# Kernel tuning notes

Hardware: AMD Instinct MI355X
Metric: run time of the kernel (lower is better)

Reference implementation:

```python
import jax, jax.numpy as jnp
import numpy as np

N, E, D, T, B, OUT = 20000, 80000, 768, 4, 3, 768
SCALE = 0.02


def _layer_norm(x, g, b):
    mu = jnp.mean(x, axis=-1, keepdims=True)
    var = jnp.var(x, axis=-1, keepdims=True)
    return (x - mu) / jnp.sqrt(var + 1e-5) * g + b


def _typed_linear(x, etype, bases, coeff):
    # DGL TypedLinear with basis regularizer: W[t] = sum_b coeff[t,b] * bases[b]
    # computed as 3 shared GEMMs + per-edge weighted sum (avoids [E,D,D] gather).
    c = coeff[etype]  # [E, B]
    y = c[:, 0:1] * (x @ bases[0])
    for bb in range(1, bases.shape[0]):
        y = y + c[:, bb:bb + 1] * (x @ bases[bb])
    return y


def _time_encode(t, freq, phase):
    return jnp.cos(t[:, None] * freq[None, :] + phase[None, :])


def _segment_softmax(scores, seg, n):
    m = jax.ops.segment_max(scores, seg, num_segments=n)
    m = jnp.where(jnp.isfinite(m), m, 0.0)  # empty segments -> -inf guard
    e = jnp.exp(scores - m[seg])
    den = jax.ops.segment_sum(e, seg, num_segments=n)[seg]
    return e / jnp.where(den == 0, 1.0, den)


def _forward(h, etime_hete, first_etime_homo, second_etime_homo, w_src, w_dst,
             ln_g, ln_b, src_bases, src_coeff, dst_bases, dst_coeff,
             user_bases, user_coeff, lin_w, lin_b, time_freq, time_phase,
             src_hete, dst_hete, first_etype_hete, src_homo, dst_homo,
             first_etype_homo, second_etype_homo, n_nodes):
    inv_sqrt_d = 1.0 / jnp.sqrt(jnp.asarray(768.0, h.dtype))
    n_src = h @ w_src.T  # src_weight (no bias)
    n_dst = h @ w_dst.T  # dst_weight (no bias)

    # --- heterogeneous edges ---
    sf = n_src[src_hete]
    df = n_dst[dst_hete]
    hete_src = jax.nn.relu(_typed_linear(_layer_norm(sf, ln_g, ln_b), first_etype_hete, src_bases, src_coeff))
    msg_h = _time_encode(etime_hete, time_freq, time_phase) + hete_src
    e_h = jnp.sum(msg_h * df, axis=1) * inv_sqrt_d
    a_h = _segment_softmax(e_h, dst_hete, n_nodes)
    h_hete = jax.ops.segment_sum(a_h[:, None] * msg_h, dst_hete, num_segments=n_nodes)

    # --- homogeneous edges ---
    sf = n_src[src_homo]
    df = n_dst[dst_homo]
    dst_feat = jax.nn.relu(_typed_linear(_layer_norm(df, ln_g, ln_b), first_etype_homo, dst_bases, dst_coeff))
    homo_feat = jax.nn.relu(_typed_linear(_layer_norm(sf, ln_g, ln_b), second_etype_homo, user_bases, user_coeff))
    t_homo = jnp.maximum(first_etime_homo, second_etime_homo)
    msg_o = _time_encode(t_homo, time_freq, time_phase) + homo_feat
    e_o = jnp.sum(msg_o * dst_feat, axis=1) * inv_sqrt_d
    a_o = _segment_softmax(e_o, dst_homo, n_nodes)
    h_homo = jax.ops.segment_sum(a_o[:, None] * msg_o, dst_homo, num_segments=n_nodes)

    n = jnp.concatenate([h_hete, h_homo], axis=-1)  # [N, 2D]
    z = jax.nn.relu(n @ lin_w.T + lin_b)
    zn = jnp.linalg.norm(z, axis=1, keepdims=True)
    return z / jnp.where(zn == 0, 1.0, zn)


def setup_inputs() -> dict:
    key = jax.random.key(0)
    ks = jax.random.split(key, 24)
    inp = {
        'h': jax.random.normal(ks[0], (N, D), jnp.float32),
        'etime_hete': jax.random.uniform(ks[1], (E,), jnp.float32),
        'first_etime_homo': jax.random.uniform(ks[2], (E,), jnp.float32),
        'second_etime_homo': jax.random.uniform(ks[3], (E,), jnp.float32),
        'w_src': jax.random.normal(ks[4], (D, D), jnp.float32) * SCALE,
        'w_dst': jax.random.normal(ks[5], (D, D), jnp.float32) * SCALE,
        'ln_g': jnp.ones((D,), jnp.float32),
        'ln_b': jnp.zeros((D,), jnp.float32),
        'src_bases': jax.random.normal(ks[6], (B, D, D), jnp.float32) * SCALE,
        'src_coeff': jax.random.normal(ks[7], (T, B), jnp.float32),
        'dst_bases': jax.random.normal(ks[8], (B, D, D), jnp.float32) * SCALE,
        'dst_coeff': jax.random.normal(ks[9], (T, B), jnp.float32),
        'user_bases': jax.random.normal(ks[10], (B, D, D), jnp.float32) * SCALE,
        'user_coeff': jax.random.normal(ks[11], (T, B), jnp.float32),
        'lin_w': jax.random.normal(ks[12], (OUT, 2 * D), jnp.float32) * SCALE,
        'lin_b': jnp.zeros((OUT,), jnp.float32),
        'time_freq': jnp.asarray(1.0 / 10 ** np.linspace(0, 9, D), jnp.float32),
        'time_phase': jnp.zeros((D,), jnp.float32),
        'src_hete': jax.random.randint(ks[13], (E,), 0, N, jnp.int32),
        'dst_hete': jax.random.randint(ks[14], (E,), 0, N, jnp.int32),
        'first_etype_hete': jax.random.randint(ks[15], (E,), 0, T, jnp.int32),
        'src_homo': jax.random.randint(ks[16], (E,), 0, N, jnp.int32),
        'dst_homo': jax.random.randint(ks[17], (E,), 0, N, jnp.int32),
        'first_etype_homo': jax.random.randint(ks[18], (E,), 0, T, jnp.int32),
        'second_etype_homo': jax.random.randint(ks[19], (E,), 0, T, jnp.int32),
        'num_nodes': N,
    }
    return inp


def reference(h, etime_hete, first_etime_homo, second_etime_homo, w_src, w_dst,
              ln_g, ln_b, src_bases, src_coeff, dst_bases, dst_coeff,
              user_bases, user_coeff, lin_w, lin_b, time_freq, time_phase,
              src_hete, dst_hete, first_etype_hete, src_homo, dst_homo,
              first_etype_homo, second_etype_homo, num_nodes):
    return _forward(h, etime_hete, first_etime_homo, second_etime_homo, w_src,
                    w_dst, ln_g, ln_b, src_bases, src_coeff, dst_bases,
                    dst_coeff, user_bases, user_coeff, lin_w, lin_b,
                    time_freq, time_phase, src_hete, dst_hete,
                    first_etype_hete, src_homo, dst_homo, first_etype_homo,
                    second_etype_homo, num_nodes)
```

## Files before the change

### kernel.cpp

```cpp
#include <hip/hip_runtime.h>
#include <hip/hip_bf16.h>
#include <stdint.h>

#define D 768
#define INV_SQRT_D 0.03608439182435161269f

static void* g_scratch = nullptr;
#define SCRATCH_BYTES ((size_t)600 * 1024 * 1024)

__attribute__((constructor))
static void _alloc_scratch() {
    if (hipMalloc(&g_scratch, SCRATCH_BYTES) != hipSuccess) g_scratch = nullptr;
}

static inline int cdiv(int a, int b) { return (a + b - 1) / b; }

typedef __attribute__((ext_vector_type(8))) short bf16x8;
typedef __attribute__((ext_vector_type(4))) float f32x4;

__device__ __forceinline__ unsigned short f2b(float f) {
    union { float f; unsigned u; } c; c.f = f;
    unsigned r = c.u + 0x7FFF + ((c.u >> 16) & 1);
    return (unsigned short)(r >> 16);
}
__device__ __forceinline__ float b2f(unsigned short u) {
    union { unsigned u; float f; } c; c.u = (unsigned)u << 16;
    return c.f;
}

__device__ __forceinline__ float block_reduce_sum(float v) {
#pragma unroll
    for (int off = 32; off > 0; off >>= 1) v += __shfl_down(v, off, 64);
    __shared__ float sm[4];
    int lane = threadIdx.x & 63, w = threadIdx.x >> 6;
    __syncthreads();
    if (lane == 0) sm[w] = v;
    __syncthreads();
    return (sm[0] + sm[1]) + (sm[2] + sm[3]);
}

template <bool CONCAT, bool BF16C, bool RELU, bool BIAS>
__global__ __launch_bounds__(256) void mfma_gemm(
    const unsigned short* __restrict__ A1, const unsigned short* __restrict__ A2,
    int lda, int ksplit,
    const unsigned short* __restrict__ B, int ldb,
    void* __restrict__ Cv, int ldc,
    const float* __restrict__ bias,
    int M, int K)
{
    __shared__ unsigned short As[128 * 32];
    __shared__ unsigned short Bs[128 * 32];
    const int tid = threadIdx.x;
    const int wv = tid >> 6, lane = tid & 63;
    const int m0 = blockIdx.y * 128, n0 = blockIdx.x * 128;
    const int wm = (wv >> 1) << 6;
    const int wn = (wv & 1) << 6;
    const int fr = lane & 15;
    const int fq = lane >> 4;

    f32x4 acc[4][4] = {};

    for (int k0 = 0; k0 < K; k0 += 32) {
        const unsigned short* Asrc = A1;
        int kk = k0;
        if (CONCAT && k0 >= ksplit) { Asrc = A2; kk = k0 - ksplit; }
#pragma unroll
        for (int j = 0; j < 2; ++j) {
            int idx = j * 256 + tid;
            int row = idx >> 2, cb = (idx & 3) << 3;
            int am = m0 + row; if (am > M - 1) am = M - 1;
            const unsigned short* ga = Asrc + (size_t)am * lda + kk + cb;
            char* la = (char*)As + (size_t)(j * 256 + wv * 64) * 16;
            __builtin_amdgcn_global_load_lds(
                (const __attribute__((address_space(1))) unsigned int*)ga,
                (__attribute__((address_space(3))) unsigned int*)la, 16, 0, 0);
            const unsigned short* gb = B + (size_t)(n0 + row) * ldb + k0 + cb;
            char* lb = (char*)Bs + (size_t)(j * 256 + wv * 64) * 16;
            __builtin_amdgcn_global_load_lds(
                (const __attribute__((address_space(1))) unsigned int*)gb,
                (__attribute__((address_space(3))) unsigned int*)lb, 16, 0, 0);
        }
        __syncthreads();

        bf16x8 af[4], bfv[4];
#pragma unroll
        for (int i = 0; i < 4; ++i) {
            af[i]  = *(const bf16x8*)&As[(wm + i * 16 + fr) * 32 + fq * 8];
            bfv[i] = *(const bf16x8*)&Bs[(wn + i * 16 + fr) * 32 + fq * 8];
        }
#pragma unroll
        for (int mi = 0; mi < 4; ++mi)
#pragma unroll
            for (int ni = 0; ni < 4; ++ni)
                acc[mi][ni] = __builtin_amdgcn_mfma_f32_16x16x32_bf16(
                    af[mi], bfv[ni], acc[mi][ni], 0, 0, 0);
        __syncthreads();
    }

#pragma unroll
    for (int mi = 0; mi < 4; ++mi) {
#pragma unroll
        for (int r = 0; r < 4; ++r) {
            int m = m0 + wm + mi * 16 + fq * 4 + r;
            if (m >= M) continue;
#pragma unroll
            for (int ni = 0; ni < 4; ++ni) {
                int n = n0 + wn + ni * 16 + fr;
                float v = acc[mi][ni][r];
                if (BIAS) v += bias[n];
                if (RELU) v = fmaxf(v, 0.f);
                if (BF16C) ((unsigned short*)Cv)[(size_t)m * ldc + n] = f2b(v);
                else       ((float*)Cv)[(size_t)m * ldc + n] = v;
            }
        }
    }
}

__global__ void f32_to_bf16_kernel(const float* __restrict__ in,
                                   unsigned short* __restrict__ out, int n4) {
    int i = blockIdx.x * 256 + threadIdx.x;
    if (i >= n4) return;
    float4 v = *reinterpret_cast<const float4*>(in + (size_t)i * 4);
    ushort4 o;
    o.x = f2b(v.x); o.y = f2b(v.y); o.z = f2b(v.z); o.w = f2b(v.w);
    *reinterpret_cast<ushort4*>(out + (size_t)i * 4) = o;
}

__global__ __launch_bounds__(256) void combine_transpose_kernel(
    const float* __restrict__ in, const float* __restrict__ coeff,
    unsigned short* __restrict__ out) {
    int t = blockIdx.z;
    float c0 = coeff[t * 3 + 0], c1 = coeff[t * 3 + 1], c2 = coeff[t * 3 + 2];
    __shared__ float tile[32][33];
    int bx = blockIdx.x * 32, by = blockIdx.y * 32;
    int tx = threadIdx.x & 31, ty = threadIdx.x >> 5;
#pragma unroll
    for (int i = 0; i < 32; i += 8) {
        size_t idx = (size_t)(by + ty + i) * D + bx + tx;
        tile[ty + i][tx] = c0 * in[idx] + c1 * in[idx + (size_t)D * D]
                         + c2 * in[idx + (size_t)2 * D * D];
    }
    __syncthreads();
    unsigned short* o = out + (size_t)t * D * D;
#pragma unroll
    for (int i = 0; i < 32; i += 8)
        o[(size_t)(bx + ty + i) * D + by + tx] = f2b(tile[tx][ty + i]);
}

__global__ __launch_bounds__(256) void ln_bf16_kernel(
    unsigned short* __restrict__ x, int ld,
    const float* __restrict__ g, const float* __restrict__ b)
{
    unsigned short* r = x + (size_t)blockIdx.x * ld;
    int t = threadIdx.x;
    float v0 = b2f(r[t]), v1 = b2f(r[t + 256]), v2 = b2f(r[t + 512]);
    float s = block_reduce_sum(v0 + v1 + v2);
    float mu = s * (1.f / 768.f);
    float d0 = v0 - mu, d1 = v1 - mu, d2 = v2 - mu;
    float q = block_reduce_sum(d0 * d0 + d1 * d1 + d2 * d2);
    float rstd = 1.f / sqrtf(q * (1.f / 768.f) + 1e-5f);
    r[t]       = f2b(d0 * rstd * g[t]       + b[t]);
    r[t + 256] = f2b(d1 * rstd * g[t + 256] + b[t + 256]);
    r[t + 512] = f2b(d2 * rstd * g[t + 512] + b[t + 512]);
}

__global__ __launch_bounds__(256) void score_hete_kernel(
    const unsigned short* __restrict__ P, int ldp,
    const unsigned short* __restrict__ nd, int ldn,
    const float* __restrict__ etime,
    const int* __restrict__ src, const int* __restrict__ dst, const int* __restrict__ et,
    const float* __restrict__ freq, const float* __restrict__ phase,
    float* __restrict__ esc, int E)
{
    int e = blockIdx.x * 4 + (threadIdx.x >> 6);
    if (e >= E) return;
    int l = threadIdx.x & 63;
    int s = src[e], d = dst[e], ty = et[e];
    float tv = etime[e];
    const unsigned short* ps = P + (size_t)s * ldp + ty * D;
    const unsigned short* pd = nd + (size_t)d * ldn;
    float acc = 0.f;
    {
        bf16x8 a = *(const bf16x8*)(ps + l * 8);
        bf16x8 b = *(const bf16x8*)(pd + l * 8);
#pragma unroll
        for (int q = 0; q < 8; ++q) {
            int j = l * 8 + q;
            float m = __cosf(tv * freq[j] + phase[j]) + b2f((unsigned short)a[q]);
            acc += m * b2f((unsigned short)b[q]);
        }
    }
    if (l < 32) {
        bf16x8 a = *(const bf16x8*)(ps + 512 + l * 8);
        bf16x8 b = *(const bf16x8*)(pd + 512 + l * 8);
#pragma unroll
        for (int q = 0; q < 8; ++q) {
            int j = 512 + l * 8 + q;
            float m = __cosf(tv * freq[j] + phase[j]) + b2f((unsigned short)a[q]);
            acc += m * b2f((unsigned short)b[q]);
        }
    }
#pragma unroll
    for (int off = 32; off > 0; off >>= 1) acc += __shfl_down(acc, off, 64);
    if (l == 0) esc[e] = acc * INV_SQRT_D;
}

__global__ __launch_bounds__(256) void score_homo_kernel(
    const unsigned short* __restrict__ Pd, int ldpd,
    const unsigned short* __restrict__ Pu, int ldpu,
    const float* __restrict__ t1, const float* __restrict__ t2,
    const int* __restrict__ src, const int* __restrict__ dst,
    const int* __restrict__ et1, const int* __restrict__ et2,
    const float* __restrict__ freq, const float* __restrict__ phase,
    float* __restrict__ esc, int E)
{
    int e = blockIdx.x * 4 + (threadIdx.x >> 6);
    if (e >= E) return;
    int l = threadIdx.x & 63;
    int s = src[e], d = dst[e];
    int ta = et1[e], tb = et2[e];
    float tv = fmaxf(t1[e], t2[e]);
    const unsigned short* pu = Pu + (size_t)s * ldpu + tb * D;
    const unsigned short* pd = Pd + (size_t)d * ldpd + ta * D;
    float acc = 0.f;
    {
        bf16x8 a = *(const bf16x8*)(pu + l * 8);
        bf16x8 b = *(const bf16x8*)(pd + l * 8);
#pragma unroll
        for (int q = 0; q < 8; ++q) {
            int j = l * 8 + q;
            float m = __cosf(tv * freq[j] + phase[j]) + b2f((unsigned short)a[q]);
            acc += m * b2f((unsigned short)b[q]);
        }
    }
    if (l < 32) {
        bf16x8 a = *(const bf16x8*)(pu + 512 + l * 8);
        bf16x8 b = *(const bf16x8*)(pd + 512 + l * 8);
#pragma unroll
        for (int q = 0; q < 8; ++q) {
            int j = 512 + l * 8 + q;
            float m = __cosf(tv * freq[j] + phase[j]) + b2f((unsigned short)a[q]);
            acc += m * b2f((unsigned short)b[q]);
        }
    }
#pragma unroll
    for (int off = 32; off > 0; off >>= 1) acc += __shfl_down(acc, off, 64);
    if (l == 0) esc[e] = acc * INV_SQRT_D;
}

__global__ void zero_int_kernel(int* __restrict__ p, int n) {
    int i = blockIdx.x * 256 + threadIdx.x;
    if (i < n) p[i] = 0;
}

__global__ void count_kernel(const int* __restrict__ dst, int* __restrict__ cnt, int E) {
    int e = blockIdx.x * 256 + threadIdx.x;
    if (e < E) atomicAdd(&cnt[dst[e]], 1);
}

__global__ __launch_bounds__(1024) void scan_kernel(
    const int* __restrict__ cnt, int* __restrict__ offs, int n)
{
    __shared__ int tmp[1024];
    __shared__ int carry;
    int tid = threadIdx.x;
    if (tid == 0) carry = 0;
    __syncthreads();
    for (int base = 0; base < n; base += 1024) {
        int idx = base + tid;
        int v = (idx < n) ? cnt[idx] : 0;
        tmp[tid] = v;
        __syncthreads();
        for (int off = 1; off < 1024; off <<= 1) {
            int t = (tid >= off) ? tmp[tid - off] : 0;
            __syncthreads();
            tmp[tid] += t;
            __syncthreads();
        }
        int inc = tmp[tid];
        int c = carry;
        if (idx < n) offs[idx] = c + inc - v;
        __syncthreads();
        if (tid == 0) carry = c + tmp[1023];
        __syncthreads();
    }
    if (tid == 0) offs[n] = carry;
}

__global__ void scatter_kernel(const int* __restrict__ dst, const int* __restrict__ offs,
                               int* __restrict__ cur, int* __restrict__ list, int E) {
    int e = blockIdx.x * 256 + threadIdx.x;
    if (e < E) {
        int d = dst[e];
        int pos = offs[d] + atomicAdd(&cur[d], 1);
        list[pos] = e;
    }
}

__global__ void seg_softmax_kernel(const int* __restrict__ offs, const int* __restrict__ list,
                                   float* __restrict__ score, int n) {
    int v = blockIdx.x * 256 + threadIdx.x;
    if (v >= n) return;
    int a = offs[v], b = offs[v + 1];
    if (a == b) return;
    float m = -INFINITY;
    for (int i = a; i < b; i++) m = fmaxf(m, score[list[i]]);
    float den = 0.f;
    for (int i = a; i < b; i++) den += expf(score[list[i]] - m);
    float inv = 1.f / den;
    for (int i = a; i < b; i++) { int e = list[i]; score[e] = expf(score[e] - m) * inv; }
}

__global__ __launch_bounds__(256) void agg_hete_kernel(
    const int* __restrict__ offs, const int* __restrict__ list,
    const float* __restrict__ a,
    const unsigned short* __restrict__ P, int ldp,
    const float* __restrict__ etime,
    const int* __restrict__ src, const int* __restrict__ et,
    const float* __restrict__ freq, const float* __restrict__ phase,
    unsigned short* __restrict__ out)
{
    int v = blockIdx.x;
    int t = threadIdx.x;
    float f0 = freq[t], f1 = freq[t + 256], f2 = freq[t + 512];
    float p0 = phase[t], p1 = phase[t + 256], p2 = phase[t + 512];
    float a0 = 0.f, a1 = 0.f, a2 = 0.f;
    for (int i = offs[v]; i < offs[v + 1]; ++i) {
        int e = list[i];
        int s = src[e], ty = et[e];
        float w = a[e];
        float tv = etime[e];
        const unsigned short* ps = P + (size_t)s * ldp + ty * D;
        a0 += w * (__cosf(tv * f0 + p0) + b2f(ps[t]));
        a1 += w * (__cosf(tv * f1 + p1) + b2f(ps[t + 256]));
        a2 += w * (__cosf(tv * f2 + p2) + b2f(ps[t + 512]));
    }
    unsigned short* o = out + (size_t)v * D;
    o[t] = f2b(a0); o[t + 256] = f2b(a1); o[t + 512] = f2b(a2);
}

__global__ __launch_bounds__(256) void agg_homo_kernel(
    const int* __restrict__ offs, const int* __restrict__ list,
    const float* __restrict__ a,
    const unsigned short* __restrict__ Pu, int ldpu,
    const float* __restrict__ t1, const float* __restrict__ t2,
    const int* __restrict__ src, const int* __restrict__ et2,
    const float* __restrict__ freq, const float* __restrict__ phase,
    unsigned short* __restrict__ out)
{
    int v = blockIdx.x;
    int t = threadIdx.x;
    float f0 = freq[t], f1 = freq[t + 256], f2 = freq[t + 512];
    float p0 = phase[t], p1 = phase[t + 256], p2 = phase[t + 512];
    float a0 = 0.f, a1 = 0.f, a2 = 0.f;
    for (int i = offs[v]; i < offs[v + 1]; ++i) {
        int e = list[i];
        int s = src[e], tb = et2[e];
        float w = a[e];
        float tv = fmaxf(t1[e], t2[e]);
        const unsigned short* pu = Pu + (size_t)s * ldpu + tb * D;
        a0 += w * (__cosf(tv * f0 + p0) + b2f(pu[t]));
        a1 += w * (__cosf(tv * f1 + p1) + b2f(pu[t + 256]));
        a2 += w * (__cosf(tv * f2 + p2) + b2f(pu[t + 512]));
    }
    unsigned short* o = out + (size_t)v * D;
    o[t] = f2b(a0); o[t + 256] = f2b(a1); o[t + 512] = f2b(a2);
}

__global__ __launch_bounds__(256) void normalize_kernel(
    const float* __restrict__ z, float* __restrict__ out)
{
    const float* x = z + (size_t)blockIdx.x * D;
    int t = threadIdx.x;
    float v0 = x[t], v1 = x[t + 256], v2 = x[t + 512];
    float s = block_reduce_sum(v0 * v0 + v1 * v1 + v2 * v2);
    float nrm = sqrtf(s);
    float inv = (nrm == 0.f) ? 1.f : 1.f / nrm;
    float* o = out + (size_t)blockIdx.x * D;
    o[t] = v0 * inv; o[t + 256] = v1 * inv; o[t + 512] = v2 * inv;
}

__global__ void fill_f32_kernel(float* __restrict__ p, float v, int n) {
    int i = blockIdx.x * 256 + threadIdx.x;
    if (i < n) p[i] = v;
}

extern "C" void kernel_launch(void* const* d_in, const int* in_sizes, int n_in,
                              void* d_out, int out_size, void* d_ws, size_t ws_size,
                              hipStream_t stream)
{
    const float* h          = (const float*)d_in[0];
    const float* etime_hete = (const float*)d_in[1];
    const float* t1_homo    = (const float*)d_in[2];
    const float* t2_homo    = (const float*)d_in[3];
    const float* w_src      = (const float*)d_in[4];
    const float* w_dst      = (const float*)d_in[5];
    const float* ln_g       = (const float*)d_in[6];
    const float* ln_b       = (const float*)d_in[7];
    const float* src_bases  = (const float*)d_in[8];
    const float* src_coeff  = (const float*)d_in[9];
    const float* dst_bases  = (const float*)d_in[10];
    const float* dst_coeff  = (const float*)d_in[11];
    const float* user_bases = (const float*)d_in[12];
    const float* user_coeff = (const float*)d_in[13];
    const float* lin_w      = (const float*)d_in[14];
    const float* lin_b      = (const float*)d_in[15];
    const float* time_freq  = (const float*)d_in[16];
    const float* time_phase = (const float*)d_in[17];
    const int* src_hete = (const int*)d_in[18];
    const int* dst_hete = (const int*)d_in[19];
    const int* et_hete  = (const int*)d_in[20];
    const int* src_homo = (const int*)d_in[21];
    const int* dst_homo = (const int*)d_in[22];
    const int* et1_homo = (const int*)d_in[23];
    const int* et2_homo = (const int*)d_in[24];

    const int N = in_sizes[0] / D;
    const int E = in_sizes[1];

    const size_t szST  = (size_t)N * 1536 * 2;
    const size_t szPSU = (size_t)N * 6144 * 2;
    const size_t szPD  = (size_t)N * 3072 * 2;
    const size_t szVb  = (size_t)N * D * 2;
    const size_t szW   = (size_t)D * D * 2;
    size_t need = szST + szPSU + szPD + 3 * szVb
                + 2 * szW + 2 * szW + 8 * szW + 4 * szW
                + (size_t)E * 4 + (size_t)N * 4
                + (((size_t)(N + 1) * 4 + 255) & ~(size_t)255) + (size_t)E * 4 + 8192;

    char* base;
    if (ws_size >= need) base = (char*)d_ws;
    else if (g_scratch)  base = (char*)g_scratch;
    else {
        fill_f32_kernel<<<cdiv(out_size, 256), 256, 0, stream>>>(
            (float*)d_out, 1000.0f + (float)(ws_size >> 20), out_size);
        return;
    }

    char* p = base;
    auto carve = [&](size_t bytes) { char* r = p; p += (bytes + 255) & ~(size_t)255; return r; };
    unsigned short* STb = (unsigned short*)carve(szST);
    unsigned short* PSU = (unsigned short*)carve(szPSU);
    unsigned short* PD  = (unsigned short*)carve(szPD);
    unsigned short* hb  = (unsigned short*)carve(szVb);
    unsigned short* hAb = (unsigned short*)carve(szVb);
    unsigned short* hOb = (unsigned short*)carve(szVb);
    unsigned short* wsb = (unsigned short*)carve(2 * szW);
    unsigned short* lwb = (unsigned short*)carve(2 * szW);
    unsigned short* suW = (unsigned short*)carve(8 * szW);
    unsigned short* dstW = (unsigned short*)carve(4 * szW);
    float* esc = (float*)carve((size_t)E * 4);
    int* cnt   = (int*)carve((size_t)N * 4);
    int* offs  = (int*)carve((size_t)(N + 1) * 4);
    int* list  = (int*)carve((size_t)E * 4);
    float* z   = (float*)PSU;

    unsigned short* Sb = STb;
    unsigned short* Tb = STb + 768;
    unsigned short* Psrc_t  = PSU;
    unsigned short* Puser_t = PSU + 3072;

    const int eb = cdiv(E, 256), nb = cdiv(N, 256);
    const int MB = cdiv(N, 128);
    dim3 g_proj(12, MB);
    dim3 g_psu(48, MB);
    dim3 g_pd(24, MB);
    dim3 g_fin(6, MB);
    dim3 ct_grid(24, 24, 4);
    const int seb = cdiv(E, 4);

    f32_to_bf16_kernel<<<cdiv(N * D / 4, 256), 256, 0, stream>>>(h, hb, N * D / 4);
    f32_to_bf16_kernel<<<cdiv(D * D / 4, 256), 256, 0, stream>>>(w_src, wsb, D * D / 4);
    f32_to_bf16_kernel<<<cdiv(D * D / 4, 256), 256, 0, stream>>>(w_dst, wsb + (size_t)D * D, D * D / 4);
    f32_to_bf16_kernel<<<cdiv(D * 2 * D / 4, 256), 256, 0, stream>>>(lin_w, lwb, D * 2 * D / 4);
    combine_transpose_kernel<<<ct_grid, 256, 0, stream>>>(src_bases, src_coeff, suW);
    combine_transpose_kernel<<<ct_grid, 256, 0, stream>>>(user_bases, user_coeff, suW + (size_t)4 * D * D);
    combine_transpose_kernel<<<ct_grid, 256, 0, stream>>>(dst_bases, dst_coeff, dstW);

    mfma_gemm<false, true, false, false><<<g_proj, 256, 0, stream>>>(
        hb, hb, D, D, wsb, D, STb, 1536, nullptr, N, D);
    ln_bf16_kernel<<<N, 256, 0, stream>>>(Sb, 1536, ln_g, ln_b);

    mfma_gemm<false, true, true, false><<<g_psu, 256, 0, stream>>>(
        Sb, Sb, 1536, D, suW, D, PSU, 6144, nullptr, N, D);

    zero_int_kernel<<<nb, 256, 0, stream>>>(cnt, N);
    count_kernel<<<eb, 256, 0, stream>>>(dst_hete, cnt, E);
    scan_kernel<<<1, 1024, 0, stream>>>(cnt, offs, N);
    zero_int_kernel<<<nb, 256, 0, stream>>>(cnt, N);
    scatter_kernel<<<eb, 256, 0, stream>>>(dst_hete, offs, cnt, list, E);

    score_hete_kernel<<<seb, 256, 0, stream>>>(Psrc_t, 6144, Tb, 1536, etime_hete,
                                               src_hete, dst_hete, et_hete,
                                               time_freq, time_phase, esc, E);
    seg_softmax_kernel<<<nb, 256, 0, stream>>>(offs, list, esc, N);
    agg_hete_kernel<<<N, 256, 0, stream>>>(offs, list, esc, Psrc_t, 6144, etime_hete,
                                           src_hete, et_hete, time_freq, time_phase, hAb);

    ln_bf16_kernel<<<N, 256, 0, stream>>>(Tb, 1536, ln_g, ln_b);
    mfma_gemm<false, true, true, false><<<g_pd, 256, 0, stream>>>(
        Tb, Tb, 1536, D, dstW, D, PD, 3072, nullptr, N, D);

    zero_int_kernel<<<nb, 256, 0, stream>>>(cnt, N);
    count_kernel<<<eb, 256, 0, stream>>>(dst_homo, cnt, E);
    scan_kernel<<<1, 1024, 0, stream>>>(cnt, offs, N);
    zero_int_kernel<<<nb, 256, 0, stream>>>(cnt, N);
    scatter_kernel<<<eb, 256, 0, stream>>>(dst_homo, offs, cnt, list, E);

    score_homo_kernel<<<seb, 256, 0, stream>>>(PD, 3072, Puser_t, 6144,
                                               t1_homo, t2_homo, src_homo, dst_homo,
                                               et1_homo, et2_homo, time_freq, time_phase, esc, E);
    seg_softmax_kernel<<<nb, 256, 0, stream>>>(offs, list, esc, N);
    agg_homo_kernel<<<N, 256, 0, stream>>>(offs, list, esc, Puser_t, 6144,
                                           t1_homo, t2_homo, src_homo, et2_homo,
                                           time_freq, time_phase, hOb);

    mfma_gemm<true, false, true, true><<<g_fin, 256, 0, stream>>>(
        hAb, hOb, D, D, lwb, 2 * D, z, D, lin_b, N, 2 * D);
    normalize_kernel<<<N, 256, 0, stream>>>(z, (float*)d_out);
}
```

Baseline: 1.142 ms.

## Use wave-per-node vectorized aggregation and merge both CSR builds

Result: no change. 1.127 ms (-1.3%).

```diff
diff --git a/kernel.cpp b/kernel.cpp
--- a/kernel.cpp
+++ b/kernel.cpp
@@ -18,10 +18,13 @@
 typedef __attribute__((ext_vector_type(8))) short bf16x8;
 typedef __attribute__((ext_vector_type(4))) float f32x4;
 
+__device__ __forceinline__ unsigned cvt2b(float lo, float hi) {
+    unsigned r;
+    asm("v_cvt_pk_bf16_f32 %0, %1, %2" : "=v"(r) : "v"(lo), "v"(hi));
+    return r;
+}
 __device__ __forceinline__ unsigned short f2b(float f) {
-    union { float f; unsigned u; } c; c.f = f;
-    unsigned r = c.u + 0x7FFF + ((c.u >> 16) & 1);
-    return (unsigned short)(r >> 16);
+    return (unsigned short)cvt2b(f, f);
 }
 __device__ __forceinline__ float b2f(unsigned short u) {
     union { unsigned u; float f; } c; c.u = (unsigned)u << 16;
@@ -253,47 +256,61 @@
     if (i < n) p[i] = 0;
 }
 
-__global__ void count_kernel(const int* __restrict__ dst, int* __restrict__ cnt, int E) {
+__global__ void count2_kernel(const int* __restrict__ dA, const int* __restrict__ dB,
+                              int* __restrict__ cntA, int* __restrict__ cntB, int E) {
     int e = blockIdx.x * 256 + threadIdx.x;
-    if (e < E) atomicAdd(&cnt[dst[e]], 1);
-}
-
-__global__ __launch_bounds__(1024) void scan_kernel(
-    const int* __restrict__ cnt, int* __restrict__ offs, int n)
+    if (e < E) {
+        atomicAdd(&cntA[dA[e]], 1);
+        atomicAdd(&cntB[dB[e]], 1);
+    }
+}
+
+__global__ __launch_bounds__(1024) void scan2_kernel(
+    const int* __restrict__ cntA, int* __restrict__ offsA,
+    const int* __restrict__ cntB, int* __restrict__ offsB, int n)
 {
     __shared__ int tmp[1024];
     __shared__ int carry;
     int tid = threadIdx.x;
-    if (tid == 0) carry = 0;
-    __syncthreads();
-    for (int base = 0; base < n; base += 1024) {
-        int idx = base + tid;
-        int v = (idx < n) ? cnt[idx] : 0;
-        tmp[tid] = v;
+    for (int g = 0; g < 2; ++g) {
+        const int* cnt = g ? cntB : cntA;
+        int* offs = g ? offsB : offsA;
         __syncthreads();
-        for (int off = 1; off < 1024; off <<= 1) {
-            int t = (tid >= off) ? tmp[tid - off] : 0;
+        if (tid == 0) carry = 0;
+        __syncthreads();
+        for (int base = 0; base < n; base += 1024) {
+            int idx = base + tid;
+            int v = (idx < n) ? cnt[idx] : 0;
+            tmp[tid] = v;
             __syncthreads();
-            tmp[tid] += t;
+            for (int off = 1; off < 1024; off <<= 1) {
+                int t = (tid >= off) ? tmp[tid - off] : 0;
+                __syncthreads();
+                tmp[tid] += t;
+                __syncthreads();
+            }
+            int inc = tmp[tid];
+            int c = carry;
+            if (idx < n) offs[idx] = c + inc - v;
             __syncthreads();
-        }
-        int inc = tmp[tid];
-        int c = carry;
-        if (idx < n) offs[idx] = c + inc - v;
-        __syncthreads();
-        if (tid == 0) carry = c + tmp[1023];
-        __syncthreads();
-    }
-    if (tid == 0) offs[n] = carry;
-}
-
-__global__ void scatter_kernel(const int* __restrict__ dst, const int* __restrict__ offs,
-                               int* __restrict__ cur, int* __restrict__ list, int E) {
+            if (tid == 0) carry = c + tmp[1023];
+            __syncthreads();
+        }
+        if (tid == 0) offs[n] = carry;
+    }
+}
+
+__global__ void scatter2_kernel(
+    const int* __restrict__ dA, const int* __restrict__ offsA,
+    int* __restrict__ curA, int* __restrict__ listA,
+    const int* __restrict__ dB, const int* __restrict__ offsB,
+    int* __restrict__ curB, int* __restrict__ listB, int E) {
     int e = blockIdx.x * 256 + threadIdx.x;
     if (e < E) {
-        int d = dst[e];
-        int pos = offs[d] + atomicAdd(&cur[d], 1);
-        list[pos] = e;
+        int d = dA[e];
+        listA[offsA[d] + atomicAdd(&curA[d], 1)] = e;
+        d = dB[e];
+        listB[offsB[d] + atomicAdd(&curB[d], 1)] = e;
     }
 }
 
@@ -311,60 +328,74 @@
     for (int i = a; i < b; i++) { int e = list[i]; score[e] = expf(score[e] - m) * inv; }
 }
 
-__global__ __launch_bounds__(256) void agg_hete_kernel(
+template <bool IS_HOMO>
+__global__ __launch_bounds__(256) void agg_kernel(
     const int* __restrict__ offs, const int* __restrict__ list,
     const float* __restrict__ a,
     const unsigned short* __restrict__ P, int ldp,
-    const float* __restrict__ etime,
+    const float* __restrict__ t1, const float* __restrict__ t2,
     const int* __restrict__ src, const int* __restrict__ et,
     const float* __restrict__ freq, const float* __restrict__ phase,
-    unsigned short* __restrict__ out)
-{
-    int v = blockIdx.x;
-    int t = threadIdx.x;
-    float f0 = freq[t], f1 = freq[t + 256], f2 = freq[t + 512];
-    float p0 = phase[t], p1 = phase[t + 256], p2 = phase[t + 512];
-    float a0 = 0.f, a1 = 0.f, a2 = 0.f;
-    for (int i = offs[v]; i < offs[v + 1]; ++i) {
+    unsigned short* __restrict__ out, int nN)
+{
+    int v = blockIdx.x * 4 + (threadIdx.x >> 6);
+    if (v >= nN) return;
+    int l = threadIdx.x & 63;
+
+    float frq[16], phs[16], acc[16];
+#pragma unroll
+    for (int q = 0; q < 16; ++q) { frq[q] = 0.f; phs[q] = 0.f; acc[q] = 0.f; }
+    {
+        float4 f0 = *(const float4*)(freq + l * 8);
+        float4 f1 = *(const float4*)(freq + l * 8 + 4);
+        float4 p0 = *(const float4*)(phase + l * 8);
+        float4 p1 = *(const float4*)(phase + l * 8 + 4);
+        frq[0] = f0.x; frq[1] = f0.y; frq[2] = f0.z; frq[3] = f0.w;
+        frq[4] = f1.x; frq[5] = f1.y; frq[6] = f1.z; frq[7] = f1.w;
+        phs[0] = p0.x; phs[1] = p0.y; phs[2] = p0.z; phs[3] = p0.w;
+        phs[4] = p1.x; phs[5] = p1.y; phs[6] = p1.z; phs[7] = p1.w;
+    }
+    if (l < 32) {
+        float4 f0 = *(const float4*)(freq + 512 + l * 8);
+        float4 f1 = *(const float4*)(freq + 512 + l * 8 + 4);
+        float4 p0 = *(const float4*)(phase + 512 + l * 8);
+        float4 p1 = *(const float4*)(phase + 512 + l * 8 + 4);
+        frq[8]  = f0.x; frq[9]  = f0.y; frq[10] = f0.z; frq[11] = f0.w;
+        frq[12] = f1.x; frq[13] = f1.y; frq[14] = f1.z; frq[15] = f1.w;
+        phs[8]  = p0.x; phs[9]  = p0.y; phs[10] = p0.z; phs[11] = p0.w;
+        phs[12] = p1.x; phs[13] = p1.y; phs[14] = p1.z; phs[15] = p1.w;
+    }
+
+    int i0 = offs[v], i1 = offs[v + 1];
+    for (int i = i0; i < i1; ++i) {
         int e = list[i];
         int s = src[e], ty = et[e];
         float w = a[e];
-        float tv = etime[e];
+        float tv = IS_HOMO ? fmaxf(t1[e], t2[e]) : t1[e];
         const unsigned short* ps = P + (size_t)s * ldp + ty * D;
-        a0 += w * (__cosf(tv * f0 + p0) + b2f(ps[t]));
-        a1 += w * (__cosf(tv * f1 + p1) + b2f(ps[t + 256]));
-        a2 += w * (__cosf(tv * f2 + p2) + b2f(ps[t + 512]));
-    }
+        bf16x8 r0 = *(const bf16x8*)(ps + l * 8);
+#pragma unroll
+        for (int q = 0; q < 8; ++q)
+            acc[q] += w * (__cosf(tv * frq[q] + phs[q]) + b2f((unsigned short)r0[q]));
+        if (l < 32) {
+            bf16x8 r1 = *(const bf16x8*)(ps + 512 + l * 8);
+#pragma unroll
+            for (int q = 0; q < 8; ++q)
+                acc[8 + q] += w * (__cosf(tv * frq[8 + q] + phs[8 + q])
+                                   + b2f((unsigned short)r1[q]));
+        }
+    }
+
     unsigned short* o = out + (size_t)v * D;
-    o[t] = f2b(a0); o[t + 256] = f2b(a1); o[t + 512] = f2b(a2);
-}
-
-__global__ __launch_bounds__(256) void agg_homo_kernel(
-    const int* __restrict__ offs, const int* __restrict__ list,
-    const float* __restrict__ a,
-    const unsigned short* __restrict__ Pu, int ldpu,
-    const float* __restrict__ t1, const float* __restrict__ t2,
-    const int* __restrict__ src, const int* __restrict__ et2,
-    const float* __restrict__ freq, const float* __restrict__ phase,
-    unsigned short* __restrict__ out)
-{
-    int v = blockIdx.x;
-    int t = threadIdx.x;
-    float f0 = freq[t], f1 = freq[t + 256], f2 = freq[t + 512];
-    float p0 = phase[t], p1 = phase[t + 256], p2 = phase[t + 512];
-    float a0 = 0.f, a1 = 0.f, a2 = 0.f;
-    for (int i = offs[v]; i < offs[v + 1]; ++i) {
-        int e = list[i];
-        int s = src[e], tb = et2[e];
-        float w = a[e];
-        float tv = fmaxf(t1[e], t2[e]);
-        const unsigned short* pu = Pu + (size_t)s * ldpu + tb * D;
-        a0 += w * (__cosf(tv * f0 + p0) + b2f(pu[t]));
-        a1 += w * (__cosf(tv * f1 + p1) + b2f(pu[t + 256]));
-        a2 += w * (__cosf(tv * f2 + p2) + b2f(pu[t + 512]));
-    }
-    unsigned short* o = out + (size_t)v * D;
-    o[t] = f2b(a0); o[t + 256] = f2b(a1); o[t + 512] = f2b(a2);
+    uint4 st;
+    st.x = cvt2b(acc[0], acc[1]); st.y = cvt2b(acc[2], acc[3]);
+    st.z = cvt2b(acc[4], acc[5]); st.w = cvt2b(acc[6], acc[7]);
+    *reinterpret_cast<uint4*>(o + (size_t)l * 8) = st;
+    if (l < 32) {
+        st.x = cvt2b(acc[8], acc[9]);   st.y = cvt2b(acc[10], acc[11]);
+        st.z = cvt2b(acc[12], acc[13]); st.w = cvt2b(acc[14], acc[15]);
+        *reinterpret_cast<uint4*>(o + 512 + (size_t)l * 8) = st;
+    }
 }
 
 __global__ __launch_bounds__(256) void normalize_kernel(
@@ -425,8 +456,9 @@
     const size_t szW   = (size_t)D * D * 2;
     size_t need = szST + szPSU + szPD + 3 * szVb
                 + 2 * szW + 2 * szW + 8 * szW + 4 * szW
-                + (size_t)E * 4 + (size_t)N * 4
-                + (((size_t)(N + 1) * 4 + 255) & ~(size_t)255) + (size_t)E * 4 + 8192;
+                + (size_t)E * 4 + (size_t)2 * N * 4
+                + 2 * (((size_t)(N + 1) * 4 + 255) & ~(size_t)255)
+                + (size_t)2 * E * 4 + 16384;
 
     char* base;
     if (ws_size >= need) base = (char*)d_ws;
@@ -449,18 +481,21 @@
     unsigned short* lwb = (unsigned short*)carve(2 * szW);
     unsigned short* suW = (unsigned short*)carve(8 * szW);
     unsigned short* dstW = (unsigned short*)carve(4 * szW);
-    float* esc = (float*)carve((size_t)E * 4);
-    int* cnt   = (int*)carve((size_t)N * 4);
-    int* offs  = (int*)carve((size_t)(N + 1) * 4);
-    int* list  = (int*)carve((size_t)E * 4);
-    float* z   = (float*)PSU;
+    float* esc  = (float*)carve((size_t)E * 4);
+    int* cnt    = (int*)carve((size_t)2 * N * 4);
+    int* offsA  = (int*)carve((size_t)(N + 1) * 4);
+    int* offsB  = (int*)carve((size_t)(N + 1) * 4);
+    int* listA  = (int*)carve((size_t)E * 4);
+    int* listB  = (int*)carve((size_t)E * 4);
+    float* z    = (float*)PSU;
 
     unsigned short* Sb = STb;
     unsigned short* Tb = STb + 768;
     unsigned short* Psrc_t  = PSU;
     unsigned short* Puser_t = PSU + 3072;
 
-    const int eb = cdiv(E, 256), nb = cdiv(N, 256);
+    const int eb = cdiv(E, 256);
+    const int nb2 = cdiv(2 * N, 256);
     const int MB = cdiv(N, 128);
     dim3 g_proj(12, MB);
     dim3 g_psu(48, MB);
@@ -468,6 +503,7 @@
     dim3 g_fin(6, MB);
     dim3 ct_grid(24, 24, 4);
     const int seb = cdiv(E, 4);
+    const int agb = cdiv(N, 4);
 
     f32_to_bf16_kernel<<<cdiv(N * D / 4, 256), 256, 0, stream>>>(h, hb, N * D / 4);
     f32_to_bf16_kernel<<<cdiv(D * D / 4, 256), 256, 0, stream>>>(w_src, wsb, D * D / 4);
@@ -477,6 +513,13 @@
     combine_transpose_kernel<<<ct_grid, 256, 0, stream>>>(user_bases, user_coeff, suW + (size_t)4 * D * D);
     combine_transpose_kernel<<<ct_grid, 256, 0, stream>>>(dst_bases, dst_coeff, dstW);
 
+    zero_int_kernel<<<nb2, 256, 0, stream>>>(cnt, 2 * N);
+    count2_kernel<<<eb, 256, 0, stream>>>(dst_hete, dst_homo, cnt, cnt + N, E);
+    scan2_kernel<<<1, 1024, 0, stream>>>(cnt, offsA, cnt + N, offsB, N);
+    zero_int_kernel<<<nb2, 256, 0, stream>>>(cnt, 2 * N);
+    scatter2_kernel<<<eb, 256, 0, stream>>>(dst_hete, offsA, cnt, listA,
+                                            dst_homo, offsB, cnt + N, listB, E);
+
     mfma_gemm<false, true, false, false><<<g_proj, 256, 0, stream>>>(
         hb, hb, D, D, wsb, D, STb, 1536, nullptr, N, D);
     ln_bf16_kernel<<<N, 256, 0, stream>>>(Sb, 1536, ln_g, ln_b);
@@ -484,36 +527,25 @@
     mfma_gemm<false, true, true, false><<<g_psu, 256, 0, stream>>>(
         Sb, Sb, 1536, D, suW, D, PSU, 6144, nullptr, N, D);
 
-    zero_int_kernel<<<nb, 256, 0, stream>>>(cnt, N);
-    count_kernel<<<eb, 256, 0, stream>>>(dst_hete, cnt, E);
-    scan_kernel<<<1, 1024, 0, stream>>>(cnt, offs, N);
-    zero_int_kernel<<<nb, 256, 0, stream>>>(cnt, N);
-    scatter_kernel<<<eb, 256, 0, stream>>>(dst_hete, offs, cnt, list, E);
-
     score_hete_kernel<<<seb, 256, 0, stream>>>(Psrc_t, 6144, Tb, 1536, etime_hete,
                                                src_hete, dst_hete, et_hete,
                                                time_freq, time_phase, esc, E);
-    seg_softmax_kernel<<<nb, 256, 0, stream>>>(offs, list, esc, N);
-    agg_hete_kernel<<<N, 256, 0, stream>>>(offs, list, esc, Psrc_t, 6144, etime_hete,
-                                           src_hete, et_hete, time_freq, time_phase, hAb);
+    seg_softmax_kernel<<<cdiv(N, 256), 256, 0, stream>>>(offsA, listA, esc, N);
+    agg_kernel<false><<<agb, 256, 0, stream>>>(offsA, listA, esc, Psrc_t, 6144,
+                                               etime_hete, nullptr, src_hete, et_hete,
+                                               time_freq, time_phase, hAb, N);
 
     ln_bf16_kernel<<<N, 256, 0, stream>>>(Tb, 1536, ln_g, ln_b);
     mfma_gemm<false, true, true, false><<<g_pd, 256, 0, stream>>>(
         Tb, Tb, 1536, D, dstW, D, PD, 3072, nullptr, N, D);
 
-    zero_int_kernel<<<nb, 256, 0, stream>>>(cnt, N);
-    count_kernel<<<eb, 256, 0, stream>>>(dst_homo, cnt, E);
-    scan_kernel<<<1, 1024, 0, stream>>>(cnt, offs, N);
-    zero_int_kernel<<<nb, 256, 0, stream>>>(cnt, N);
-    scatter_kernel<<<eb, 256, 0, stream>>>(dst_homo, offs, cnt, list, E);
-
     score_homo_kernel<<<seb, 256, 0, stream>>>(PD, 3072, Puser_t, 6144,
                                                t1_homo, t2_homo, src_homo, dst_homo,
                                                et1_homo, et2_homo, time_freq, time_phase, esc, E);
-    seg_softmax_kernel<<<nb, 256, 0, stream>>>(offs, list, esc, N);
-    agg_homo_kernel<<<N, 256, 0, stream>>>(offs, list, esc, Puser_t, 6144,
-                                           t1_homo, t2_homo, src_homo, et2_homo,
-                                           time_freq, time_phase, hOb);
+    seg_softmax_kernel<<<cdiv(N, 256), 256, 0, stream>>>(offsB, listB, esc, N);
+    agg_kernel<true><<<agb, 256, 0, stream>>>(offsB, listB, esc, Puser_t, 6144,
+                                              t1_homo, t2_homo, src_homo, et2_homo,
+                                              time_freq, time_phase, hOb, N);
 
     mfma_gemm<true, false, true, true><<<g_fin, 256, 0, stream>>>(
         hAb, hOb, D, D, lwb, 2 * D, z, D, lin_b, N, 2 * D);
```
